# Optimization experiments

Hardware: AMD Instinct MI355X
Metric: run time of the kernel (lower is better)

## Reference

```python
import jax, jax.numpy as jnp
import numpy as np

B = 8192
I_SIZE = 1024
H_SIZE = 1024
C2 = 2.7183  # module's hard-coded e approximation

def setup_inputs() -> dict:
    key = jax.random.key(0)
    k0, k1, k2, k3, k4 = jax.random.split(key, 5)
    input_tensor = jax.random.uniform(k0, (B, I_SIZE + 1), dtype=jnp.float32)  # last col = dt >= 0
    h_cur = jax.random.normal(k1, (B, H_SIZE), dtype=jnp.float32)
    c_cur = jax.random.normal(k2, (B, H_SIZE), dtype=jnp.float32)
    W_layers = jax.random.normal(k3, (4 * H_SIZE, I_SIZE + H_SIZE), dtype=jnp.float32) * 0.02
    b_layers = jnp.zeros((4 * H_SIZE,), dtype=jnp.float32)
    W_desc = jax.random.normal(k4, (H_SIZE, H_SIZE), dtype=jnp.float32) * 0.02
    b_desc = jnp.zeros((H_SIZE,), dtype=jnp.float32)
    return {"input_tensor": input_tensor, "h_cur": h_cur, "c_cur": c_cur,
            "W_layers": W_layers, "b_layers": b_layers,
            "W_desc": W_desc, "b_desc": b_desc}

def reference(input_tensor, h_cur, c_cur, W_layers, b_layers, W_desc, b_desc):
    x = input_tensor[:, :-1]          # [B, I]
    dt = input_tensor[:, -1:]         # [B, 1]
    # map_elapse_time: T = 1/log(t + e), broadcast over h_size (matmul with ones == broadcast)
    T = 1.0 / jnp.log(dt + C2)        # [B, 1]
    C_ST = jnp.tanh(h_cur @ W_desc.T + b_desc)          # [B, H]
    h_adj = h_cur - C_ST + T * C_ST                     # decayed short-term memory
    combined = jnp.concatenate([x, h_adj], axis=1)      # [B, I+H]
    gates = combined @ W_layers.T + b_layers            # [B, 4H]
    cc_i, cc_f, cc_o, cc_g = jnp.split(gates, 4, axis=1)
    i = jax.nn.sigmoid(cc_i)
    f = jax.nn.sigmoid(cc_f)
    o = jax.nn.sigmoid(cc_o)
    g = jnp.tanh(cc_g)
    c_next = f * c_cur + i * g
    h_next = o * jnp.tanh(c_next)
    return (h_next, c_next)
```

## Files before the change

### kernel.cpp

```cpp
#include <hip/hip_runtime.h>
#include <hip/hip_bf16.h>
#include <math.h>

typedef __bf16 bf16x8 __attribute__((ext_vector_type(8)));
typedef float  f32x4  __attribute__((ext_vector_type(4)));

#define B_ROWS 8192
#define HSZ    1024

#define GLOAD16(gsrc, ldst)                                                          \
  __builtin_amdgcn_global_load_lds((const __attribute__((address_space(1))) void*)(gsrc), \
                                   (__attribute__((address_space(3))) void*)(ldst),  \
                                   16, 0, 0)

__device__ inline unsigned short f2bf(float f) {
  union { float f; unsigned u; } x; x.f = f;
  unsigned r = x.u + 0x7fffu + ((x.u >> 16) & 1u);
  return (unsigned short)(r >> 16);
}

__device__ inline float sigm(float x) { return 1.0f / (1.0f + __expf(-x)); }

__global__ void k_convert(const float* __restrict__ inp,
                          const float* __restrict__ h,
                          const float* __restrict__ Wl,
                          const float* __restrict__ Wd,
                          unsigned short* __restrict__ comb,
                          unsigned short* __restrict__ Wlb,
                          unsigned short* __restrict__ hb,
                          unsigned short* __restrict__ Wdb,
                          float* __restrict__ Tm1) {
  const long stride = (long)gridDim.x * blockDim.x;
  const long tid0 = (long)blockIdx.x * blockDim.x + threadIdx.x;

#define CNV8(dst, s0, s1) { ushort4 u0, u1;                                   \
    u0.x = f2bf(s0.x); u0.y = f2bf(s0.y); u0.z = f2bf(s0.z); u0.w = f2bf(s0.w); \
    u1.x = f2bf(s1.x); u1.y = f2bf(s1.y); u1.z = f2bf(s1.z); u1.w = f2bf(s1.w); \
    *(ushort4*)(dst) = u0; *(ushort4*)((dst) + 4) = u1; }

  for (long i = tid0; i < (long)B_ROWS * HSZ / 8; i += stride) {
    float4 v0 = ((const float4*)h)[i * 2], v1 = ((const float4*)h)[i * 2 + 1];
    CNV8(hb + i * 8, v0, v1);
  }
  for (long i = tid0; i < (long)B_ROWS * HSZ / 8; i += stride) {
    long e = i * 8; long b = e >> 10; long c = e & 1023;
    const float* s = inp + b * 1025 + c;
    float4 v0 = *(const float4*)s, v1 = *(const float4*)(s + 4);
    CNV8(comb + b * 2048 + c, v0, v1);
  }
  for (long i = tid0; i < 4096L * 2048 / 8; i += stride) {
    float4 v0 = ((const float4*)Wl)[i * 2], v1 = ((const float4*)Wl)[i * 2 + 1];
    CNV8(Wlb + i * 8, v0, v1);
  }
  for (long i = tid0; i < 1024L * 1024 / 8; i += stride) {
    float4 v0 = ((const float4*)Wd)[i * 2], v1 = ((const float4*)Wd)[i * 2 + 1];
    CNV8(Wdb + i * 8, v0, v1);
  }
  for (long i = tid0; i < B_ROWS; i += stride) {
    float dt = inp[i * 1025 + 1024];
    Tm1[i] = 1.0f / logf(dt + 2.7183f) - 1.0f;
  }
#undef CNV8
}

__global__ void k_gemm1(const unsigned short* __restrict__ A,
                        const unsigned short* __restrict__ Bm,
                        const float* __restrict__ h,
                        const float* __restrict__ bd,
                        const float* __restrict__ Tm1,
                        unsigned short* __restrict__ comb) {
  const int K = 1024;
  __shared__ __align__(16) unsigned short As[128 * 32];
  __shared__ __align__(16) unsigned short Bs[128 * 32];
  const int tid = threadIdx.x;
  const int lane = tid & 63;
  const int wave = tid >> 6;
  const int wr = wave >> 1, wc = wave & 1;
  const int bRow = blockIdx.x;
  const int bCol = blockIdx.y;

  const int sRow = tid >> 2;
  const int sK = (tid & 3) * 8;
  const unsigned short* aSrc0 = A + (long)(bRow * 128 + sRow) * K + sK;
  const unsigned short* aSrc1 = A + (long)(bRow * 128 + 64 + sRow) * K + sK;
  const unsigned short* bSrc0 = Bm + (long)(bCol * 128 + sRow) * K + sK;
  const unsigned short* bSrc1 = Bm + (long)(bCol * 128 + 64 + sRow) * K + sK;
  unsigned short* aDst0 = As + tid * 8;
  unsigned short* aDst1 = As + 2048 + tid * 8;
  unsigned short* bDst0 = Bs + tid * 8;
  unsigned short* bDst1 = Bs + 2048 + tid * 8;

  f32x4 acc[4][4] = {};
  const int fr = lane & 15, fk = (lane >> 4) * 8;

  for (int k0 = 0; k0 < K; k0 += 32) {
    GLOAD16(aSrc0 + k0, aDst0);
    GLOAD16(aSrc1 + k0, aDst1);
    GLOAD16(bSrc0 + k0, bDst0);
    GLOAD16(bSrc1 + k0, bDst1);
    __syncthreads();
    bf16x8 a[4], b[4];
#pragma unroll
    for (int m = 0; m < 4; m++) a[m] = *(const bf16x8*)(As + (wr * 64 + m * 16 + fr) * 32 + fk);
#pragma unroll
    for (int n = 0; n < 4; n++) b[n] = *(const bf16x8*)(Bs + (wc * 64 + n * 16 + fr) * 32 + fk);
#pragma unroll
    for (int m = 0; m < 4; m++)
#pragma unroll
      for (int n = 0; n < 4; n++)
        acc[m][n] = __builtin_amdgcn_mfma_f32_16x16x32_bf16(a[m], b[n], acc[m][n], 0, 0, 0);
    __syncthreads();
  }

  const int cr = (lane >> 4) * 4;
  const int cc = lane & 15;
#pragma unroll
  for (int m = 0; m < 4; m++)
#pragma unroll
    for (int n = 0; n < 4; n++) {
      const int col = bCol * 128 + wc * 64 + n * 16 + cc;
#pragma unroll
      for (int r = 0; r < 4; r++) {
        const int row = bRow * 128 + wr * 64 + m * 16 + cr + r;
        float v = acc[m][n][r] + bd[col];
        float cst = tanhf(v);
        float hadj = h[(long)row * HSZ + col] + Tm1[row] * cst;
        comb[(long)row * 2048 + 1024 + col] = f2bf(hadj);
      }
    }
}

#define NT2 64
__global__ __launch_bounds__(512, 2)
void k_gemm2_ww(const unsigned short* __restrict__ A,
                const unsigned short* __restrict__ Bm,
                const float* __restrict__ bl,
                const float* __restrict__ c_cur,
                float* __restrict__ out) {
  __shared__ __align__(16) unsigned short lds[4][16384];

  const int tid = threadIdx.x;
  const int lane = tid & 63;
  const int wid = tid >> 6;
  const int wr = wid >> 2;
  const int wc = wid & 3;

  const int bid = blockIdx.x;
  const int xcd = bid & 7;
  const int ii = bid >> 3;
  const int sweep = ii >> 5;
  const int pos = ii & 31;
  const int bRow = xcd * 4 + sweep * 2 + (pos & 1);
  const int bCol = pos >> 1;

  const int sr = tid >> 2;
  const int swsel = (sr >> 1) & 3;
  const int gk = ((tid & 3) ^ swsel) << 3;
  const unsigned short* aBase = A + (long)(bRow * 256 + sr) * 2048 + gk;
  const int rl0 = sr, rl1 = 128 + sr;
  const int grow0 = ((rl0 >> 4) & 3) * 1024 + bCol * 64 + (rl0 >> 6) * 16 + (rl0 & 15);
  const int grow1 = ((rl1 >> 4) & 3) * 1024 + bCol * 64 + (rl1 >> 6) * 16 + (rl1 & 15);
  const unsigned short* bBase0 = Bm + (long)grow0 * 2048 + gk;
  const unsigned short* bBase1 = Bm + (long)grow1 * 2048 + gk;

#define STAGE_A2(slot, tt) { unsigned short* d_ = &lds[slot][0] + tid * 8;        \
    GLOAD16(aBase + (long)(tt) * 32, d_);                                          \
    GLOAD16(aBase + 128L * 2048 + (long)(tt) * 32, d_ + 512 * 8); }
#define STAGE_B2(slot, tt) { unsigned short* d_ = &lds[slot][8192] + tid * 8;     \
    GLOAD16(bBase0 + (long)(tt) * 32, d_);                                         \
    GLOAD16(bBase1 + (long)(tt) * 32, d_ + 512 * 8); }

  const int fr = lane & 15, q = lane >> 4;
  int offA[8], offB[4];
#pragma unroll
  for (int m = 0; m < 8; m++) {
    const int row = wr * 128 + m * 16 + fr;
    offA[m] = row * 32 + ((q ^ ((row >> 1) & 3)) << 3);
  }
#pragma unroll
  for (int n = 0; n < 4; n++) {
    const int row = wc * 64 + n * 16 + fr;
    offB[n] = 8192 + row * 32 + ((q ^ ((row >> 1) & 3)) << 3);
  }

  f32x4 acc[8][4] = {};

#define BODY(t, SLOT)                                                                \
  {                                                                                  \
    if ((t) + 2 < NT2) { STAGE_A2((SLOT) ^ 2, (t) + 2); STAGE_B2((SLOT) ^ 2, (t) + 2); } \
    const unsigned short* buf = &lds[SLOT][0];                                       \
    bf16x8 aF[8], bF[4];                                                             \
    _Pragma("unroll")                                                                \
    for (int n = 0; n < 4; n++) bF[n] = *(const bf16x8*)(buf + offB[n]);             \
    _Pragma("unroll")                                                                \
    for (int m = 0; m < 8; m++) aF[m] = *(const bf16x8*)(buf + offA[m]);             \
    __builtin_amdgcn_s_setprio(1);                                                   \
    _Pragma("unroll")                                                                \
    for (int m = 0; m < 8; m++)                                                      \
      _Pragma("unroll")                                                              \
      for (int n = 0; n < 4; n++)                                                    \
        acc[m][n] = __builtin_amdgcn_mfma_f32_16x16x32_bf16(aF[m], bF[n], acc[m][n], 0, 0, 0); \
    __builtin_amdgcn_s_setprio(0);                                                   \
  }
#define IBOUND() { asm volatile("s_waitcnt vmcnt(0)" ::: "memory"); __builtin_amdgcn_s_barrier(); }

  STAGE_A2(0, 0); STAGE_B2(0, 0);
  STAGE_A2(1, 1); STAGE_B2(1, 1);
  IBOUND();

  for (int ip = 0; ip < 16; ++ip) {
    const int t0 = ip * 4;
    BODY(t0,     0); BODY(t0 + 1, 1); IBOUND();
    BODY(t0 + 2, 2); BODY(t0 + 3, 3); IBOUND();
  }
#undef BODY
#undef IBOUND

  const int cr = (lane >> 4) * 4;
  const int cc = lane & 15;
  const int j = bCol * 64 + wc * 16 + cc;
#pragma unroll
  for (int m = 0; m < 8; m++) {
#pragma unroll
    for (int r = 0; r < 4; r++) {
      const int row = bRow * 256 + wr * 128 + m * 16 + cr + r;
      float iv = sigm(acc[m][0][r] + bl[j]);
      float fv = sigm(acc[m][1][r] + bl[1024 + j]);
      float ov = sigm(acc[m][2][r] + bl[2048 + j]);
      float gv = tanhf(acc[m][3][r] + bl[3072 + j]);
      float cn = fv * c_cur[(long)row * HSZ + j] + iv * gv;
      float hn = ov * tanhf(cn);
      out[(long)row * HSZ + j] = hn;
      out[(long)B_ROWS * HSZ + (long)row * HSZ + j] = cn;
    }
  }
}

extern "C" void kernel_launch(void* const* d_in, const int* in_sizes, int n_in,
                              void* d_out, int out_size, void* d_ws, size_t ws_size,
                              hipStream_t stream) {
  const float* inp = (const float*)d_in[0];
  const float* h   = (const float*)d_in[1];
  const float* c   = (const float*)d_in[2];
  const float* Wl  = (const float*)d_in[3];
  const float* bl  = (const float*)d_in[4];
  const float* Wd  = (const float*)d_in[5];
  const float* bd  = (const float*)d_in[6];

  char* ws = (char*)d_ws;
  unsigned short* comb = (unsigned short*)(ws);
  unsigned short* Wlb  = (unsigned short*)(ws + 33554432);
  unsigned short* hb   = (unsigned short*)(ws + 50331648);
  unsigned short* Wdb  = (unsigned short*)(ws + 67108864);
  float*          Tm1  = (float*)(ws + 69206016);
  float*          out  = (float*)d_out;

  hipLaunchKernelGGL(k_convert, dim3(2048), dim3(256), 0, stream,
                     inp, h, Wl, Wd, comb, Wlb, hb, Wdb, Tm1);
  hipLaunchKernelGGL(k_gemm1, dim3(64, 8), dim3(256), 0, stream,
                     hb, Wdb, h, bd, Tm1, comb);
  hipLaunchKernelGGL(k_gemm2_ww, dim3(512), dim3(512), 0, stream,
                     comb, Wlb, bl, c, out);
}
```

Baseline: 228.1 us.

## Use 4 big waves per block with 128x128 warp tiles and 3-deep prefetch

The second GEMM kernel changes from 8 waves (64x64 per wave) to 4 waves per block, each computing a 128x128 sub-tile with an 8x8 accumulator array, so fragment reuse per LDS read doubles. The load pipeline moves from paired double-buffer barriers to a per-step barrier with three tiles in flight across four LDS slots, waiting only on older loads through vmcnt. The larger accumulator sharply raises register pressure, and launch bounds drop to one block per SM. With fewer waves there is less latency hiding.

```diff
diff --git a/kernel.cpp b/kernel.cpp
--- a/kernel.cpp
+++ b/kernel.cpp
@@ -131,8 +131,8 @@
 }
 
 #define NT2 64
-__global__ __launch_bounds__(512, 2)
-void k_gemm2_ww(const unsigned short* __restrict__ A,
+__global__ __launch_bounds__(256, 1)
+void k_gemm2_bw(const unsigned short* __restrict__ A,
                 const unsigned short* __restrict__ Bm,
                 const float* __restrict__ bl,
                 const float* __restrict__ c_cur,
@@ -142,8 +142,8 @@
   const int tid = threadIdx.x;
   const int lane = tid & 63;
   const int wid = tid >> 6;
-  const int wr = wid >> 2;
-  const int wc = wid & 3;
+  const int wr = wid >> 1;
+  const int wc = wid & 1;
 
   const int bid = blockIdx.x;
   const int xcd = bid & 7;
@@ -156,82 +156,96 @@
   const int sr = tid >> 2;
   const int swsel = (sr >> 1) & 3;
   const int gk = ((tid & 3) ^ swsel) << 3;
-  const unsigned short* aBase = A + (long)(bRow * 256 + sr) * 2048 + gk;
-  const int rl0 = sr, rl1 = 128 + sr;
-  const int grow0 = ((rl0 >> 4) & 3) * 1024 + bCol * 64 + (rl0 >> 6) * 16 + (rl0 & 15);
-  const int grow1 = ((rl1 >> 4) & 3) * 1024 + bCol * 64 + (rl1 >> 6) * 16 + (rl1 & 15);
-  const unsigned short* bBase0 = Bm + (long)grow0 * 2048 + gk;
-  const unsigned short* bBase1 = Bm + (long)grow1 * 2048 + gk;
-
-#define STAGE_A2(slot, tt) { unsigned short* d_ = &lds[slot][0] + tid * 8;        \
-    GLOAD16(aBase + (long)(tt) * 32, d_);                                          \
-    GLOAD16(aBase + 128L * 2048 + (long)(tt) * 32, d_ + 512 * 8); }
-#define STAGE_B2(slot, tt) { unsigned short* d_ = &lds[slot][8192] + tid * 8;     \
-    GLOAD16(bBase0 + (long)(tt) * 32, d_);                                         \
-    GLOAD16(bBase1 + (long)(tt) * 32, d_ + 512 * 8); }
+  const unsigned short* aS0 = A + (long)(bRow * 256 +   0 + sr) * 2048 + gk;
+  const unsigned short* aS1 = A + (long)(bRow * 256 +  64 + sr) * 2048 + gk;
+  const unsigned short* aS2 = A + (long)(bRow * 256 + 128 + sr) * 2048 + gk;
+  const unsigned short* aS3 = A + (long)(bRow * 256 + 192 + sr) * 2048 + gk;
+#define GROWF(rl) (((rl) >> 4 & 3) * 1024 + bCol * 64 + ((rl) >> 6) * 16 + ((rl) & 15))
+  const unsigned short* bS0 = Bm + (long)GROWF(0   + sr) * 2048 + gk;
+  const unsigned short* bS1 = Bm + (long)GROWF(64  + sr) * 2048 + gk;
+  const unsigned short* bS2 = Bm + (long)GROWF(128 + sr) * 2048 + gk;
+  const unsigned short* bS3 = Bm + (long)GROWF(192 + sr) * 2048 + gk;
+#undef GROWF
+
+#define STG(slot, tt) { unsigned short* d_ = &lds[slot][0] + tid * 8;     \
+    GLOAD16(aS0 + (long)(tt) * 32, d_);                                    \
+    GLOAD16(aS1 + (long)(tt) * 32, d_ + 2048);                             \
+    GLOAD16(aS2 + (long)(tt) * 32, d_ + 4096);                             \
+    GLOAD16(aS3 + (long)(tt) * 32, d_ + 6144);                             \
+    GLOAD16(bS0 + (long)(tt) * 32, d_ + 8192);                             \
+    GLOAD16(bS1 + (long)(tt) * 32, d_ + 10240);                            \
+    GLOAD16(bS2 + (long)(tt) * 32, d_ + 12288);                            \
+    GLOAD16(bS3 + (long)(tt) * 32, d_ + 14336); }
 
   const int fr = lane & 15, q = lane >> 4;
-  int offA[8], offB[4];
+  int offA[8], offB[8];
 #pragma unroll
   for (int m = 0; m < 8; m++) {
     const int row = wr * 128 + m * 16 + fr;
     offA[m] = row * 32 + ((q ^ ((row >> 1) & 3)) << 3);
   }
 #pragma unroll
-  for (int n = 0; n < 4; n++) {
-    const int row = wc * 64 + n * 16 + fr;
+  for (int n = 0; n < 8; n++) {
+    const int row = wc * 128 + n * 16 + fr;
     offB[n] = 8192 + row * 32 + ((q ^ ((row >> 1) & 3)) << 3);
   }
 
-  f32x4 acc[8][4] = {};
-
-#define BODY(t, SLOT)                                                                \
+  f32x4 acc[8][8] = {};
+
+  STG(0, 0); STG(1, 1); STG(2, 2);
+
+#define BODY(t, SLOT, VM, DOSTAGE)                                                   \
   {                                                                                  \
-    if ((t) + 2 < NT2) { STAGE_A2((SLOT) ^ 2, (t) + 2); STAGE_B2((SLOT) ^ 2, (t) + 2); } \
+    asm volatile("s_waitcnt vmcnt(" #VM ")" ::: "memory");                           \
+    __builtin_amdgcn_s_barrier();                                                    \
+    if (DOSTAGE) STG(((t) + 3) & 3, (t) + 3);                                        \
     const unsigned short* buf = &lds[SLOT][0];                                       \
-    bf16x8 aF[8], bF[4];                                                             \
+    bf16x8 aF[8], bF[8];                                                             \
     _Pragma("unroll")                                                                \
-    for (int n = 0; n < 4; n++) bF[n] = *(const bf16x8*)(buf + offB[n]);             \
+    for (int n = 0; n < 8; n++) bF[n] = *(const bf16x8*)(buf + offB[n]);             \
     _Pragma("unroll")                                                                \
     for (int m = 0; m < 8; m++) aF[m] = *(const bf16x8*)(buf + offA[m]);             \
     __builtin_amdgcn_s_setprio(1);                                                   \
     _Pragma("unroll")                                                                \
     for (int m = 0; m < 8; m++)                                                      \
       _Pragma("unroll")                                                              \
-      for (int n = 0; n < 4; n++)                                                    \
+      for (int n = 0; n < 8; n++)                                                    \
         acc[m][n] = __builtin_amdgcn_mfma_f32_16x16x32_bf16(aF[m], bF[n], acc[m][n], 0, 0, 0); \
     __builtin_amdgcn_s_setprio(0);                                                   \
   }
-#define IBOUND() { asm volatile("s_waitcnt vmcnt(0)" ::: "memory"); __builtin_amdgcn_s_barrier(); }
-
-  STAGE_A2(0, 0); STAGE_B2(0, 0);
-  STAGE_A2(1, 1); STAGE_B2(1, 1);
-  IBOUND();
-
-  for (int ip = 0; ip < 16; ++ip) {
-    const int t0 = ip * 4;
-    BODY(t0,     0); BODY(t0 + 1, 1); IBOUND();
-    BODY(t0 + 2, 2); BODY(t0 + 3, 3); IBOUND();
-  }
+
+  for (int t = 0; t < 60; t += 4) {
+    BODY(t,     0, 16, true);
+    BODY(t + 1, 1, 16, true);
+    BODY(t + 2, 2, 16, true);
+    BODY(t + 3, 3, 16, true);
+  }
+  BODY(60, 0, 16, true);
+  BODY(61, 1, 16, false);
+  BODY(62, 2, 8,  false);
+  BODY(63, 3, 0,  false);
 #undef BODY
-#undef IBOUND
 
   const int cr = (lane >> 4) * 4;
   const int cc = lane & 15;
-  const int j = bCol * 64 + wc * 16 + cc;
 #pragma unroll
   for (int m = 0; m < 8; m++) {
 #pragma unroll
-    for (int r = 0; r < 4; r++) {
-      const int row = bRow * 256 + wr * 128 + m * 16 + cr + r;
-      float iv = sigm(acc[m][0][r] + bl[j]);
-      float fv = sigm(acc[m][1][r] + bl[1024 + j]);
-      float ov = sigm(acc[m][2][r] + bl[2048 + j]);
-      float gv = tanhf(acc[m][3][r] + bl[3072 + j]);
-      float cn = fv * c_cur[(long)row * HSZ + j] + iv * gv;
-      float hn = ov * tanhf(cn);
-      out[(long)row * HSZ + j] = hn;
-      out[(long)B_ROWS * HSZ + (long)row * HSZ + j] = cn;
+    for (int js = 0; js < 2; js++) {
+      const int j = bCol * 64 + (wc * 2 + js) * 16 + cc;
+      const float b0 = bl[j], b1 = bl[1024 + j], b2 = bl[2048 + j], b3 = bl[3072 + j];
+#pragma unroll
+      for (int r = 0; r < 4; r++) {
+        const int row = bRow * 256 + wr * 128 + m * 16 + cr + r;
+        float iv = sigm(acc[m][js * 4 + 0][r] + b0);
+        float fv = sigm(acc[m][js * 4 + 1][r] + b1);
+        float ov = sigm(acc[m][js * 4 + 2][r] + b2);
+        float gv = tanhf(acc[m][js * 4 + 3][r] + b3);
+        float cn = fv * c_cur[(long)row * HSZ + j] + iv * gv;
+        float hn = ov * tanhf(cn);
+        out[(long)row * HSZ + j] = hn;
+        out[(long)B_ROWS * HSZ + (long)row * HSZ + j] = cn;
+      }
     }
   }
 }
@@ -259,6 +273,6 @@
                      inp, h, Wl, Wd, comb, Wlb, hb, Wdb, Tm1);
   hipLaunchKernelGGL(k_gemm1, dim3(64, 8), dim3(256), 0, stream,
                      hb, Wdb, h, bd, Tm1, comb);
-  hipLaunchKernelGGL(k_gemm2_ww, dim3(512), dim3(512), 0, stream,
+  hipLaunchKernelGGL(k_gemm2_bw, dim3(512), dim3(256), 0, stream,
                      comb, Wlb, bl, c, out);
 }
```

New measurement: 254.9 us. +11.7%, slower.

## Register-prefetch next LDS tile and deepen global staging to three tiles ahead

Applied to the files above, without the earlier changes.

Rewrites the main loop of the second GEMM so that each iteration reads the next tile's A/B fragments from LDS into a second register set while issuing MFMAs on the current set. Global-to-LDS staging now runs three tiles ahead across four slots, and each tile waits with a partial vmcnt plus a barrier instead of a full drain every two tiles. The goal is to hide LDS read latency and global load latency behind the MFMAs. In exchange it doubles fragment register usage, which could cause spilling at 512 threads with two blocks per CU, and it adds a barrier on every tile.

```diff
diff --git a/kernel.cpp b/kernel.cpp
--- a/kernel.cpp
+++ b/kernel.cpp
@@ -132,7 +132,7 @@
 
 #define NT2 64
 __global__ __launch_bounds__(512, 2)
-void k_gemm2_ww(const unsigned short* __restrict__ A,
+void k_gemm2_rp(const unsigned short* __restrict__ A,
                 const unsigned short* __restrict__ Bm,
                 const float* __restrict__ bl,
                 const float* __restrict__ c_cur,
@@ -184,37 +184,48 @@
   }
 
   f32x4 acc[8][4] = {};
-
-#define BODY(t, SLOT)                                                                \
+  bf16x8 aC[8], bC[4], aN[8], bN[4];
+
+  STAGE_A2(0, 0); STAGE_B2(0, 0);
+  STAGE_A2(1, 1); STAGE_B2(1, 1);
+  STAGE_A2(2, 2); STAGE_B2(2, 2);
+  asm volatile("s_waitcnt vmcnt(8)" ::: "memory");
+  __builtin_amdgcn_s_barrier();
+#pragma unroll
+  for (int n = 0; n < 4; n++) bC[n] = *(const bf16x8*)(&lds[0][0] + offB[n]);
+#pragma unroll
+  for (int m = 0; m < 8; m++) aC[m] = *(const bf16x8*)(&lds[0][0] + offA[m]);
+
+#define TILE(t, aCur, bCur, aNxt, bNxt, VM, DOREAD, DOSTAGE)                         \
   {                                                                                  \
-    if ((t) + 2 < NT2) { STAGE_A2((SLOT) ^ 2, (t) + 2); STAGE_B2((SLOT) ^ 2, (t) + 2); } \
-    const unsigned short* buf = &lds[SLOT][0];                                       \
-    bf16x8 aF[8], bF[4];                                                             \
-    _Pragma("unroll")                                                                \
-    for (int n = 0; n < 4; n++) bF[n] = *(const bf16x8*)(buf + offB[n]);             \
-    _Pragma("unroll")                                                                \
-    for (int m = 0; m < 8; m++) aF[m] = *(const bf16x8*)(buf + offA[m]);             \
+    asm volatile("s_waitcnt vmcnt(" #VM ")" ::: "memory");                           \
+    __builtin_amdgcn_s_barrier();                                                    \
+    if (DOREAD) {                                                                    \
+      const unsigned short* bufN = &lds[((t) + 1) & 3][0];                           \
+      _Pragma("unroll")                                                              \
+      for (int n = 0; n < 4; n++) bNxt[n] = *(const bf16x8*)(bufN + offB[n]);        \
+      _Pragma("unroll")                                                              \
+      for (int m = 0; m < 8; m++) aNxt[m] = *(const bf16x8*)(bufN + offA[m]);        \
+    }                                                                                \
+    if (DOSTAGE) { STAGE_A2(((t) + 3) & 3, (t) + 3); STAGE_B2(((t) + 3) & 3, (t) + 3); } \
     __builtin_amdgcn_s_setprio(1);                                                   \
     _Pragma("unroll")                                                                \
     for (int m = 0; m < 8; m++)                                                      \
       _Pragma("unroll")                                                              \
       for (int n = 0; n < 4; n++)                                                    \
-        acc[m][n] = __builtin_amdgcn_mfma_f32_16x16x32_bf16(aF[m], bF[n], acc[m][n], 0, 0, 0); \
+        acc[m][n] = __builtin_amdgcn_mfma_f32_16x16x32_bf16(aCur[m], bCur[n], acc[m][n], 0, 0, 0); \
     __builtin_amdgcn_s_setprio(0);                                                   \
   }
-#define IBOUND() { asm volatile("s_waitcnt vmcnt(0)" ::: "memory"); __builtin_amdgcn_s_barrier(); }
-
-  STAGE_A2(0, 0); STAGE_B2(0, 0);
-  STAGE_A2(1, 1); STAGE_B2(1, 1);
-  IBOUND();
-
-  for (int ip = 0; ip < 16; ++ip) {
-    const int t0 = ip * 4;
-    BODY(t0,     0); BODY(t0 + 1, 1); IBOUND();
-    BODY(t0 + 2, 2); BODY(t0 + 3, 3); IBOUND();
-  }
-#undef BODY
-#undef IBOUND
+
+  for (int t = 0; t < 60; t += 2) {
+    TILE(t,     aC, bC, aN, bN, 4, true, true);
+    TILE(t + 1, aN, bN, aC, bC, 4, true, true);
+  }
+  TILE(60, aC, bC, aN, bN, 4, true,  true);
+  TILE(61, aN, bN, aC, bC, 4, true,  false);
+  TILE(62, aC, bC, aN, bN, 0, true,  false);
+  TILE(63, aN, bN, aC, bC, 0, false, false);
+#undef TILE
 
   const int cr = (lane >> 4) * 4;
   const int cc = lane & 15;
@@ -259,6 +270,6 @@
                      inp, h, Wl, Wd, comb, Wlb, hb, Wdb, Tm1);
   hipLaunchKernelGGL(k_gemm1, dim3(64, 8), dim3(256), 0, stream,
                      hb, Wdb, h, bd, Tm1, comb);
-  hipLaunchKernelGGL(k_gemm2_ww, dim3(512), dim3(512), 0, stream,
+  hipLaunchKernelGGL(k_gemm2_rp, dim3(512), dim3(512), 0, stream,
                      comb, Wlb, bl, c, out);
 }
```

Result: no change. 227.8 us (-0.1%).
